# Kernel optimization log

Measured on AMD Instinct MI355X. Metric: run time of the kernel, lower is better.

Reference implementation:

```python
import jax, jax.numpy as jnp
import numpy as np

N = 100000
E = 1600000
F_IN = 128
HID = 64


def setup_inputs() -> dict:
    key = jax.random.key(0)
    ks = jax.random.split(key, 8)
    x = jax.random.normal(ks[0], (N, F_IN), dtype=jnp.float32)
    edge_index = jax.random.randint(ks[1], (2, E), 0, N, dtype=jnp.int32)
    # GCNConv params: weight [in, out] (glorot-ish scale), bias [out]
    W1 = jax.random.normal(ks[2], (F_IN, HID), dtype=jnp.float32) / np.sqrt(F_IN)
    b1 = jnp.zeros((HID,), dtype=jnp.float32)
    W2 = jax.random.normal(ks[3], (HID, HID), dtype=jnp.float32) / np.sqrt(HID)
    b2 = jnp.zeros((HID,), dtype=jnp.float32)
    Wc = jax.random.normal(ks[4], (HID, 1), dtype=jnp.float32) / np.sqrt(HID)
    bc = jnp.zeros((1,), dtype=jnp.float32)
    return {"x": x, "edge_index": edge_index, "W1": W1, "b1": b1,
            "W2": W2, "b2": b2, "Wc": Wc, "bc": bc}


def _gcn_conv(x, src, dst, W, b):
    # PyG GCNConv: h = x @ W, then symmetric-normalized aggregation over
    # edges with self-loops: out[d] = sum_e deg^-1/2[s] deg^-1/2[d] h[s] + b
    n = x.shape[0]
    h = x @ W                                            # [N, out]
    deg = jax.ops.segment_sum(jnp.ones_like(dst, dtype=h.dtype), dst,
                              num_segments=n)            # in-degree incl. self-loops
    dinv = jnp.where(deg > 0, jax.lax.rsqrt(deg), 0.0)   # [N]
    norm = dinv[src] * dinv[dst]                         # [E+N]
    msg = h[src] * norm[:, None]                         # gather + scale
    out = jax.ops.segment_sum(msg, dst, num_segments=n)  # scatter-add
    return out + b


def reference(x, edge_index, W1, b1, W2, b2, Wc, bc):
    n = x.shape[0]
    loop = jnp.arange(n, dtype=edge_index.dtype)
    src = jnp.concatenate([edge_index[0], loop])  # add self-loops
    dst = jnp.concatenate([edge_index[1], loop])
    h = jax.nn.relu(_gcn_conv(x, src, dst, W1, b1))  # dropout in eval mode = identity
    h = jax.nn.relu(_gcn_conv(h, src, dst, W2, b2))
    return (h @ Wc + bc).squeeze(-1)  # [N]
```

## Files before the change

### kernel.cpp

```cpp
#include <hip/hip_runtime.h>


#define FIN 128
#define HIDDEN 64
#define NBUCK 196
#define CAP 9216
#define EPB 8192

typedef __attribute__((ext_vector_type(8))) short bf16x8;
typedef __attribute__((ext_vector_type(4))) float f32x4;

__device__ __forceinline__ unsigned f2bf_pair(float a, float b) {
    unsigned ua = __float_as_uint(a);
    unsigned ub = __float_as_uint(b);
    ua = (ua + 0x7FFFu + ((ua >> 16) & 1u)) >> 16;
    ub = (ub + 0x7FFFu + ((ub >> 16) & 1u)) & 0xFFFF0000u;
    return ua | ub;
}
__device__ __forceinline__ unsigned short f2bf1(float a) {
    unsigned u = __float_as_uint(a);
    return (unsigned short)((u + 0x7FFFu + ((u >> 16) & 1u)) >> 16);
}
#define BF_LO(u) __uint_as_float((u) << 16)
#define BF_HI(u) __uint_as_float((u) & 0xFFFF0000u)

__global__ __launch_bounds__(256) void k_scatter_direct(const int* __restrict__ src,
                                                        const int* __restrict__ dst,
                                                        int* __restrict__ bcursor,
                                                        int* __restrict__ pairs, int e) {
    __shared__ int h[NBUCK], base_s[NBUCK], cur[NBUCK];
    int tid = threadIdx.x;
    if (tid < NBUCK) { h[tid] = 0; cur[tid] = 0; }
    __syncthreads();
    int start = blockIdx.x * EPB;
#pragma unroll
    for (int i = 0; i < EPB / 256; i++) {
        int idx = start + tid + i * 256;
        if (idx < e) atomicAdd(&h[dst[idx] >> 9], 1);
    }
    __syncthreads();
    if (tid < NBUCK && h[tid] > 0) base_s[tid] = atomicAdd(&bcursor[tid], h[tid]);
    __syncthreads();
#pragma unroll
    for (int i = 0; i < EPB / 256; i++) {
        int idx = start + tid + i * 256;
        if (idx < e) {
            int d = dst[idx];
            int b = d >> 9;
            int pos = base_s[b] + atomicAdd(&cur[b], 1);
            if (pos < CAP) pairs[b * CAP + pos] = (src[idx] << 9) | (d & 511);
        }
    }
}

__global__ __launch_bounds__(256) void k_csr_bucket(const int* __restrict__ pairs,
                                                    const int* __restrict__ bcursor,
                                                    int2* __restrict__ rowinfo,
                                                    float* __restrict__ dinv,
                                                    int* __restrict__ csr_src, int n) {
    __shared__ int cnt[512];
    __shared__ int off[512];
    __shared__ int ws2[256];
    int tid = threadIdx.x;
    int b = blockIdx.x;
    int node0 = b << 9;
    cnt[tid] = 0; cnt[tid + 256] = 0;
    __syncthreads();
    int s0 = b * CAP;
    int s1 = s0 + min(bcursor[b], CAP);
    for (int i = s0 + tid; i < s1; i += 256) atomicAdd(&cnt[pairs[i] & 511], 1);
    __syncthreads();
    int c0 = cnt[2 * tid], c1 = cnt[2 * tid + 1];
    int tsum = c0 + c1;
    ws2[tid] = tsum;
    __syncthreads();
    for (int o = 1; o < 256; o <<= 1) {
        int x = 0;
        if (tid >= o) x = ws2[tid - o];
        __syncthreads();
        if (tid >= o) ws2[tid] += x;
        __syncthreads();
    }
    int excl = ws2[tid] - tsum;
    off[2 * tid] = excl;
    off[2 * tid + 1] = excl + c0;
    int n0 = node0 + 2 * tid, n1 = node0 + 2 * tid + 1;
    if (n0 < n) { rowinfo[n0] = make_int2(s0 + excl, c0);      dinv[n0] = rsqrtf((float)c0 + 1.0f); }
    if (n1 < n) { rowinfo[n1] = make_int2(s0 + excl + c0, c1); dinv[n1] = rsqrtf((float)c1 + 1.0f); }
    cnt[2 * tid] = 0; cnt[2 * tid + 1] = 0;
    __syncthreads();
    for (int i = s0 + tid; i < s1; i += 256) {
        int p = pairs[i];
        int l = p & 511;
        int pos = s0 + off[l] + atomicAdd(&cnt[l], 1);
        csr_src[pos] = p >> 9;
    }
}


__global__ __launch_bounds__(256) void k_mfma1(const float4* __restrict__ x4,
                                               const float* __restrict__ w1,
                                               const float* __restrict__ dinv,
                                               uint2* __restrict__ hsb, int n) {
    __shared__ unsigned short sW[64 * 136];
    int tid = threadIdx.x;
#pragma unroll
    for (int i = 0; i < 32; i++) {
        int idx = tid + i * 256;
        int k = idx >> 6, ch = idx & 63;
        sW[ch * 136 + k] = f2bf1(w1[idx]);
    }
    __syncthreads();
    int lane = tid & 63, wave = tid >> 6;
    int quad = lane >> 4, nl = lane & 15;
    int node = blockIdx.x * 64 + wave * 16 + nl;
    int ic = min(node, n - 1);
    const float4* px = x4 + (size_t)ic * 32 + quad * 2;
    bf16x8 bfr[4];
#pragma unroll
    for (int kc = 0; kc < 4; kc++) {
        float4 p = px[kc * 8];
        float4 q = px[kc * 8 + 1];
        union { unsigned u[4]; bf16x8 v; } t;
        t.u[0] = f2bf_pair(p.x, p.y); t.u[1] = f2bf_pair(p.z, p.w);
        t.u[2] = f2bf_pair(q.x, q.y); t.u[3] = f2bf_pair(q.z, q.w);
        bfr[kc] = t.v;
    }
    const bf16x8* sW8 = (const bf16x8*)sW;
    f32x4 a0 = {0.f, 0.f, 0.f, 0.f}, a1 = a0, a2 = a0, a3 = a0;
#pragma unroll
    for (int kc = 0; kc < 4; kc++) {
        int ko = kc * 4 + quad;
        bf16x8 w0 = sW8[(nl +  0) * 17 + ko];
        bf16x8 w1f = sW8[(nl + 16) * 17 + ko];
        bf16x8 w2f = sW8[(nl + 32) * 17 + ko];
        bf16x8 w3f = sW8[(nl + 48) * 17 + ko];
        a0 = __builtin_amdgcn_mfma_f32_16x16x32_bf16(w0,  bfr[kc], a0, 0, 0, 0);
        a1 = __builtin_amdgcn_mfma_f32_16x16x32_bf16(w1f, bfr[kc], a1, 0, 0, 0);
        a2 = __builtin_amdgcn_mfma_f32_16x16x32_bf16(w2f, bfr[kc], a2, 0, 0, 0);
        a3 = __builtin_amdgcn_mfma_f32_16x16x32_bf16(w3f, bfr[kc], a3, 0, 0, 0);
    }
    if (node < n) {
        float s = dinv[node];
        uint2* o = hsb + (size_t)node * 16 + quad;
        o[0]  = make_uint2(f2bf_pair(a0.x * s, a0.y * s), f2bf_pair(a0.z * s, a0.w * s));
        o[4]  = make_uint2(f2bf_pair(a1.x * s, a1.y * s), f2bf_pair(a1.z * s, a1.w * s));
        o[8]  = make_uint2(f2bf_pair(a2.x * s, a2.y * s), f2bf_pair(a2.z * s, a2.w * s));
        o[12] = make_uint2(f2bf_pair(a3.x * s, a3.y * s), f2bf_pair(a3.z * s, a3.w * s));
    }
}

__global__ __launch_bounds__(256) void k_mfma2(const float4* __restrict__ v4,
                                               const float* __restrict__ w2,
                                               const float* __restrict__ dinv,
                                               uint2* __restrict__ hsb, int n) {
    __shared__ unsigned short sW[64 * 72];
    int tid = threadIdx.x;
#pragma unroll
    for (int i = 0; i < 16; i++) {
        int idx = tid + i * 256;
        int k = idx >> 6, ch = idx & 63;
        sW[ch * 72 + k] = f2bf1(w2[idx]);
    }
    __syncthreads();
    int lane = tid & 63, wave = tid >> 6;
    int quad = lane >> 4, nl = lane & 15;
    int node = blockIdx.x * 64 + wave * 16 + nl;
    int ic = min(node, n - 1);
    const float4* px = v4 + (size_t)ic * 16 + quad * 2;
    bf16x8 bfr[2];
#pragma unroll
    for (int kc = 0; kc < 2; kc++) {
        float4 p = px[kc * 8];
        float4 q = px[kc * 8 + 1];
        union { unsigned u[4]; bf16x8 v; } t;
        t.u[0] = f2bf_pair(p.x, p.y); t.u[1] = f2bf_pair(p.z, p.w);
        t.u[2] = f2bf_pair(q.x, q.y); t.u[3] = f2bf_pair(q.z, q.w);
        bfr[kc] = t.v;
    }
    const bf16x8* sW8 = (const bf16x8*)sW;
    f32x4 a0 = {0.f, 0.f, 0.f, 0.f}, a1 = a0, a2 = a0, a3 = a0;
#pragma unroll
    for (int kc = 0; kc < 2; kc++) {
        int ko = kc * 4 + quad;
        bf16x8 w0 = sW8[(nl +  0) * 9 + ko];
        bf16x8 w1f = sW8[(nl + 16) * 9 + ko];
        bf16x8 w2f = sW8[(nl + 32) * 9 + ko];
        bf16x8 w3f = sW8[(nl + 48) * 9 + ko];
        a0 = __builtin_amdgcn_mfma_f32_16x16x32_bf16(w0,  bfr[kc], a0, 0, 0, 0);
        a1 = __builtin_amdgcn_mfma_f32_16x16x32_bf16(w1f, bfr[kc], a1, 0, 0, 0);
        a2 = __builtin_amdgcn_mfma_f32_16x16x32_bf16(w2f, bfr[kc], a2, 0, 0, 0);
        a3 = __builtin_amdgcn_mfma_f32_16x16x32_bf16(w3f, bfr[kc], a3, 0, 0, 0);
    }
    if (node < n) {
        float s = dinv[node];
        uint2* o = hsb + (size_t)node * 16 + quad;
        o[0]  = make_uint2(f2bf_pair(a0.x * s, a0.y * s), f2bf_pair(a0.z * s, a0.w * s));
        o[4]  = make_uint2(f2bf_pair(a1.x * s, a1.y * s), f2bf_pair(a1.z * s, a1.w * s));
        o[8]  = make_uint2(f2bf_pair(a2.x * s, a2.y * s), f2bf_pair(a2.z * s, a2.w * s));
        o[12] = make_uint2(f2bf_pair(a3.x * s, a3.y * s), f2bf_pair(a3.z * s, a3.w * s));
    }
}

__global__ __launch_bounds__(256) void k_agg1_fin(const int2* __restrict__ rowinfo,
                                                  const int* __restrict__ csr_src,
                                                  const uint4* __restrict__ hsb4,
                                                  const float* __restrict__ dinv,
                                                  const float4* __restrict__ b1_4,
                                                  float4* __restrict__ v4out, int n) {
    int wid = (blockIdx.x * 256 + threadIdx.x) >> 6;
    int lane = threadIdx.x & 63;
    if (wid >= n) return;
    int el = lane >> 3, cq = lane & 7;
    int2 rpd = rowinfo[wid];
    int start = rpd.x, deg = rpd.y;
    int end = start + deg;
    float4 accA = make_float4(0.f, 0.f, 0.f, 0.f), accB = accA;
    if (deg > 0) {
        int rounds = (deg + 15) >> 4;
        for (int r = 0; r < rounds; r++) {
            int e0 = start + (r << 4) + el;
            int e1 = e0 + 8;
            int s0 = csr_src[min(e0, end - 1)];
            int s1 = csr_src[min(e1, end - 1)];
            float m0 = (e0 < end) ? 1.f : 0.f;
            float m1 = (e1 < end) ? 1.f : 0.f;
            uint4 g0 = hsb4[(size_t)s0 * 8 + cq];
            uint4 g1 = hsb4[(size_t)s1 * 8 + cq];
            accA.x += m0 * BF_LO(g0.x) + m1 * BF_LO(g1.x);
            accA.y += m0 * BF_HI(g0.x) + m1 * BF_HI(g1.x);
            accA.z += m0 * BF_LO(g0.y) + m1 * BF_LO(g1.y);
            accA.w += m0 * BF_HI(g0.y) + m1 * BF_HI(g1.y);
            accB.x += m0 * BF_LO(g0.z) + m1 * BF_LO(g1.z);
            accB.y += m0 * BF_HI(g0.z) + m1 * BF_HI(g1.z);
            accB.z += m0 * BF_LO(g0.w) + m1 * BF_LO(g1.w);
            accB.w += m0 * BF_HI(g0.w) + m1 * BF_HI(g1.w);
        }
    }
#pragma unroll
    for (int off = 8; off < 64; off <<= 1) {
        accA.x += __shfl_xor(accA.x, off); accA.y += __shfl_xor(accA.y, off);
        accA.z += __shfl_xor(accA.z, off); accA.w += __shfl_xor(accA.w, off);
        accB.x += __shfl_xor(accB.x, off); accB.y += __shfl_xor(accB.y, off);
        accB.z += __shfl_xor(accB.z, off); accB.w += __shfl_xor(accB.w, off);
    }
    if (el == 0) {
        uint4 g = hsb4[(size_t)wid * 8 + cq];
        float s = dinv[wid];
        float4 bA = b1_4[cq * 2], bB = b1_4[cq * 2 + 1];
        float4 vA, vB;
        vA.x = fmaxf(s * (accA.x + BF_LO(g.x)) + bA.x, 0.f);
        vA.y = fmaxf(s * (accA.y + BF_HI(g.x)) + bA.y, 0.f);
        vA.z = fmaxf(s * (accA.z + BF_LO(g.y)) + bA.z, 0.f);
        vA.w = fmaxf(s * (accA.w + BF_HI(g.y)) + bA.w, 0.f);
        vB.x = fmaxf(s * (accB.x + BF_LO(g.z)) + bB.x, 0.f);
        vB.y = fmaxf(s * (accB.y + BF_HI(g.z)) + bB.y, 0.f);
        vB.z = fmaxf(s * (accB.z + BF_LO(g.w)) + bB.z, 0.f);
        vB.w = fmaxf(s * (accB.w + BF_HI(g.w)) + bB.w, 0.f);
        v4out[(size_t)wid * 16 + cq * 2] = vA;
        v4out[(size_t)wid * 16 + cq * 2 + 1] = vB;
    }
}

__global__ __launch_bounds__(256) void k_agg2_head(const int2* __restrict__ rowinfo,
                                                   const int* __restrict__ csr_src,
                                                   const uint4* __restrict__ hsb4,
                                                   const float* __restrict__ dinv,
                                                   const float4* __restrict__ b2_4,
                                                   const float4* __restrict__ wc_4,
                                                   const float* __restrict__ bc,
                                                   float* __restrict__ out, int n) {
    int wid = (blockIdx.x * 256 + threadIdx.x) >> 6;
    int lane = threadIdx.x & 63;
    if (wid >= n) return;
    int el = lane >> 3, cq = lane & 7;
    int2 rpd = rowinfo[wid];
    int start = rpd.x, deg = rpd.y;
    int end = start + deg;
    float4 accA = make_float4(0.f, 0.f, 0.f, 0.f), accB = accA;
    if (deg > 0) {
        int rounds = (deg + 15) >> 4;
        for (int r = 0; r < rounds; r++) {
            int e0 = start + (r << 4) + el;
            int e1 = e0 + 8;
            int s0 = csr_src[min(e0, end - 1)];
            int s1 = csr_src[min(e1, end - 1)];
            float m0 = (e0 < end) ? 1.f : 0.f;
            float m1 = (e1 < end) ? 1.f : 0.f;
            uint4 g0 = hsb4[(size_t)s0 * 8 + cq];
            uint4 g1 = hsb4[(size_t)s1 * 8 + cq];
            accA.x += m0 * BF_LO(g0.x) + m1 * BF_LO(g1.x);
            accA.y += m0 * BF_HI(g0.x) + m1 * BF_HI(g1.x);
            accA.z += m0 * BF_LO(g0.y) + m1 * BF_LO(g1.y);
            accA.w += m0 * BF_HI(g0.y) + m1 * BF_HI(g1.y);
            accB.x += m0 * BF_LO(g0.z) + m1 * BF_LO(g1.z);
            accB.y += m0 * BF_HI(g0.z) + m1 * BF_HI(g1.z);
            accB.z += m0 * BF_LO(g0.w) + m1 * BF_LO(g1.w);
            accB.w += m0 * BF_HI(g0.w) + m1 * BF_HI(g1.w);
        }
    }
#pragma unroll
    for (int off = 8; off < 64; off <<= 1) {
        accA.x += __shfl_xor(accA.x, off); accA.y += __shfl_xor(accA.y, off);
        accA.z += __shfl_xor(accA.z, off); accA.w += __shfl_xor(accA.w, off);
        accB.x += __shfl_xor(accB.x, off); accB.y += __shfl_xor(accB.y, off);
        accB.z += __shfl_xor(accB.z, off); accB.w += __shfl_xor(accB.w, off);
    }
    uint4 g = hsb4[(size_t)wid * 8 + cq];
    float s = dinv[wid];
    float4 bA = b2_4[cq * 2], bB = b2_4[cq * 2 + 1];
    float4 wA = wc_4[cq * 2], wB = wc_4[cq * 2 + 1];
    float t = fmaxf(s * (accA.x + BF_LO(g.x)) + bA.x, 0.f) * wA.x
            + fmaxf(s * (accA.y + BF_HI(g.x)) + bA.y, 0.f) * wA.y
            + fmaxf(s * (accA.z + BF_LO(g.y)) + bA.z, 0.f) * wA.z
            + fmaxf(s * (accA.w + BF_HI(g.y)) + bA.w, 0.f) * wA.w
            + fmaxf(s * (accB.x + BF_LO(g.z)) + bB.x, 0.f) * wB.x
            + fmaxf(s * (accB.y + BF_HI(g.z)) + bB.y, 0.f) * wB.y
            + fmaxf(s * (accB.z + BF_LO(g.w)) + bB.z, 0.f) * wB.z
            + fmaxf(s * (accB.w + BF_HI(g.w)) + bB.w, 0.f) * wB.w;
    t += __shfl_xor(t, 1);
    t += __shfl_xor(t, 2);
    t += __shfl_xor(t, 4);
    if (lane == 0) out[wid] = t + bc[0];
}

extern "C" void kernel_launch(void* const* d_in, const int* in_sizes, int n_in,
                              void* d_out, int out_size, void* d_ws, size_t ws_size,
                              hipStream_t stream) {
    const float* x  = (const float*)d_in[0];
    const int*   ei = (const int*)d_in[1];
    const float* W1 = (const float*)d_in[2];
    const float* b1 = (const float*)d_in[3];
    const float* W2 = (const float*)d_in[4];
    const float* b2 = (const float*)d_in[5];
    const float* Wc = (const float*)d_in[6];
    const float* bc = (const float*)d_in[7];
    int n = in_sizes[0] / FIN;
    int e = in_sizes[1] / 2;
    const int* srcv = ei;
    const int* dstv = ei + e;

    char* ws = (char*)d_ws;
    float* dinv    = (float*)(ws + 0);
    int2*  rowinfo = (int2*)(ws + (512u << 10));
    int*   csr_src = (int*)(ws + 1536u * 1024);
    int*   bcursor = (int*)(ws + 8800u * 1024);
    uint2* hsb     = (uint2*)(ws + (9u << 20));
    float* v       = (float*)(ws + (22u << 20));
    int*   pairs   = (int*)v;

    int nb_sc   = (e + EPB - 1) / EPB;
    int nb_rows = (n + 63) / 64;
    int nb_wave = (n * 64 + 255) / 256;

    hipMemsetAsync(bcursor, 0, NBUCK * sizeof(int), stream);
    k_scatter_direct<<<nb_sc, 256, 0, stream>>>(srcv, dstv, bcursor, pairs, e);
    k_csr_bucket<<<NBUCK, 256, 0, stream>>>(pairs, bcursor, rowinfo, dinv, csr_src, n);

    k_mfma1<<<nb_rows, 256, 0, stream>>>((const float4*)x, W1, dinv, hsb, n);
    k_agg1_fin<<<nb_wave, 256, 0, stream>>>(rowinfo, csr_src, (const uint4*)hsb,
                                            dinv, (const float4*)b1, (float4*)v, n);
    k_mfma2<<<nb_rows, 256, 0, stream>>>((const float4*)v, W2, dinv, hsb, n);
    k_agg2_head<<<nb_wave, 256, 0, stream>>>(rowinfo, csr_src, (const uint4*)hsb,
                                             dinv, (const float4*)b2, (const float4*)Wc,
                                             bc, (float*)d_out, n);
}
```

Measured before the change: 257.8 us.

## Map four nodes per wavefront in aggregation kernels with 16 lanes per node

Changes both aggregation kernels from one 64-lane wave per destination node to 16 lanes per node (2 edge slots × 8 feature chunks), packing four nodes per wave. This is meant to cut the masked-out lanes and the multi-level shuffle reduction that were wasted on average-degree nodes, and to launch a quarter as many blocks. In exchange each node's edge loop runs more serial rounds with less memory-level parallelism per node, and high-degree nodes cause divergence within a wave.

```diff
diff --git a/kernel.cpp b/kernel.cpp
--- a/kernel.cpp
+++ b/kernel.cpp
@@ -208,45 +208,41 @@
                                                   const float* __restrict__ dinv,
                                                   const float4* __restrict__ b1_4,
                                                   float4* __restrict__ v4out, int n) {
-    int wid = (blockIdx.x * 256 + threadIdx.x) >> 6;
     int lane = threadIdx.x & 63;
-    if (wid >= n) return;
-    int el = lane >> 3, cq = lane & 7;
-    int2 rpd = rowinfo[wid];
+    int node = (blockIdx.x * 256 + threadIdx.x) >> 4;
+    if (node >= n) return;
+    int el = (lane >> 3) & 1, cq = lane & 7;
+    int2 rpd = rowinfo[node];
     int start = rpd.x, deg = rpd.y;
     int end = start + deg;
     float4 accA = make_float4(0.f, 0.f, 0.f, 0.f), accB = accA;
-    if (deg > 0) {
-        int rounds = (deg + 15) >> 4;
-        for (int r = 0; r < rounds; r++) {
-            int e0 = start + (r << 4) + el;
-            int e1 = e0 + 8;
-            int s0 = csr_src[min(e0, end - 1)];
-            int s1 = csr_src[min(e1, end - 1)];
-            float m0 = (e0 < end) ? 1.f : 0.f;
-            float m1 = (e1 < end) ? 1.f : 0.f;
-            uint4 g0 = hsb4[(size_t)s0 * 8 + cq];
-            uint4 g1 = hsb4[(size_t)s1 * 8 + cq];
-            accA.x += m0 * BF_LO(g0.x) + m1 * BF_LO(g1.x);
-            accA.y += m0 * BF_HI(g0.x) + m1 * BF_HI(g1.x);
-            accA.z += m0 * BF_LO(g0.y) + m1 * BF_LO(g1.y);
-            accA.w += m0 * BF_HI(g0.y) + m1 * BF_HI(g1.y);
-            accB.x += m0 * BF_LO(g0.z) + m1 * BF_LO(g1.z);
-            accB.y += m0 * BF_HI(g0.z) + m1 * BF_HI(g1.z);
-            accB.z += m0 * BF_LO(g0.w) + m1 * BF_LO(g1.w);
-            accB.w += m0 * BF_HI(g0.w) + m1 * BF_HI(g1.w);
-        }
-    }
-#pragma unroll
-    for (int off = 8; off < 64; off <<= 1) {
-        accA.x += __shfl_xor(accA.x, off); accA.y += __shfl_xor(accA.y, off);
-        accA.z += __shfl_xor(accA.z, off); accA.w += __shfl_xor(accA.w, off);
-        accB.x += __shfl_xor(accB.x, off); accB.y += __shfl_xor(accB.y, off);
-        accB.z += __shfl_xor(accB.z, off); accB.w += __shfl_xor(accB.w, off);
-    }
+    int nr = (deg + 3) >> 2;
+    for (int r = 0; r < nr; r++) {
+        int base = start + (r << 2);
+        int e0 = base + el;
+        int e1 = base + 2 + el;
+        int s0 = csr_src[min(e0, end - 1)];
+        int s1 = csr_src[min(e1, end - 1)];
+        float m0 = (e0 < end) ? 1.f : 0.f;
+        float m1 = (e1 < end) ? 1.f : 0.f;
+        uint4 g0 = hsb4[(size_t)s0 * 8 + cq];
+        uint4 g1 = hsb4[(size_t)s1 * 8 + cq];
+        accA.x += m0 * BF_LO(g0.x) + m1 * BF_LO(g1.x);
+        accA.y += m0 * BF_HI(g0.x) + m1 * BF_HI(g1.x);
+        accA.z += m0 * BF_LO(g0.y) + m1 * BF_LO(g1.y);
+        accA.w += m0 * BF_HI(g0.y) + m1 * BF_HI(g1.y);
+        accB.x += m0 * BF_LO(g0.z) + m1 * BF_LO(g1.z);
+        accB.y += m0 * BF_HI(g0.z) + m1 * BF_HI(g1.z);
+        accB.z += m0 * BF_LO(g0.w) + m1 * BF_LO(g1.w);
+        accB.w += m0 * BF_HI(g0.w) + m1 * BF_HI(g1.w);
+    }
+    accA.x += __shfl_xor(accA.x, 8); accA.y += __shfl_xor(accA.y, 8);
+    accA.z += __shfl_xor(accA.z, 8); accA.w += __shfl_xor(accA.w, 8);
+    accB.x += __shfl_xor(accB.x, 8); accB.y += __shfl_xor(accB.y, 8);
+    accB.z += __shfl_xor(accB.z, 8); accB.w += __shfl_xor(accB.w, 8);
     if (el == 0) {
-        uint4 g = hsb4[(size_t)wid * 8 + cq];
-        float s = dinv[wid];
+        uint4 g = hsb4[(size_t)node * 8 + cq];
+        float s = dinv[node];
         float4 bA = b1_4[cq * 2], bB = b1_4[cq * 2 + 1];
         float4 vA, vB;
         vA.x = fmaxf(s * (accA.x + BF_LO(g.x)) + bA.x, 0.f);
@@ -257,8 +253,8 @@
         vB.y = fmaxf(s * (accB.y + BF_HI(g.z)) + bB.y, 0.f);
         vB.z = fmaxf(s * (accB.z + BF_LO(g.w)) + bB.z, 0.f);
         vB.w = fmaxf(s * (accB.w + BF_HI(g.w)) + bB.w, 0.f);
-        v4out[(size_t)wid * 16 + cq * 2] = vA;
-        v4out[(size_t)wid * 16 + cq * 2 + 1] = vB;
+        v4out[(size_t)node * 16 + cq * 2] = vA;
+        v4out[(size_t)node * 16 + cq * 2 + 1] = vB;
     }
 }
 
@@ -270,44 +266,40 @@
                                                    const float4* __restrict__ wc_4,
                                                    const float* __restrict__ bc,
                                                    float* __restrict__ out, int n) {
-    int wid = (blockIdx.x * 256 + threadIdx.x) >> 6;
     int lane = threadIdx.x & 63;
-    if (wid >= n) return;
-    int el = lane >> 3, cq = lane & 7;
-    int2 rpd = rowinfo[wid];
+    int node = (blockIdx.x * 256 + threadIdx.x) >> 4;
+    if (node >= n) return;
+    int el = (lane >> 3) & 1, cq = lane & 7;
+    int2 rpd = rowinfo[node];
     int start = rpd.x, deg = rpd.y;
     int end = start + deg;
     float4 accA = make_float4(0.f, 0.f, 0.f, 0.f), accB = accA;
-    if (deg > 0) {
-        int rounds = (deg + 15) >> 4;
-        for (int r = 0; r < rounds; r++) {
-            int e0 = start + (r << 4) + el;
-            int e1 = e0 + 8;
-            int s0 = csr_src[min(e0, end - 1)];
-            int s1 = csr_src[min(e1, end - 1)];
-            float m0 = (e0 < end) ? 1.f : 0.f;
-            float m1 = (e1 < end) ? 1.f : 0.f;
-            uint4 g0 = hsb4[(size_t)s0 * 8 + cq];
-            uint4 g1 = hsb4[(size_t)s1 * 8 + cq];
-            accA.x += m0 * BF_LO(g0.x) + m1 * BF_LO(g1.x);
-            accA.y += m0 * BF_HI(g0.x) + m1 * BF_HI(g1.x);
-            accA.z += m0 * BF_LO(g0.y) + m1 * BF_LO(g1.y);
-            accA.w += m0 * BF_HI(g0.y) + m1 * BF_HI(g1.y);
-            accB.x += m0 * BF_LO(g0.z) + m1 * BF_LO(g1.z);
-            accB.y += m0 * BF_HI(g0.z) + m1 * BF_HI(g1.z);
-            accB.z += m0 * BF_LO(g0.w) + m1 * BF_LO(g1.w);
-            accB.w += m0 * BF_HI(g0.w) + m1 * BF_HI(g1.w);
-        }
-    }
-#pragma unroll
-    for (int off = 8; off < 64; off <<= 1) {
-        accA.x += __shfl_xor(accA.x, off); accA.y += __shfl_xor(accA.y, off);
-        accA.z += __shfl_xor(accA.z, off); accA.w += __shfl_xor(accA.w, off);
-        accB.x += __shfl_xor(accB.x, off); accB.y += __shfl_xor(accB.y, off);
-        accB.z += __shfl_xor(accB.z, off); accB.w += __shfl_xor(accB.w, off);
-    }
-    uint4 g = hsb4[(size_t)wid * 8 + cq];
-    float s = dinv[wid];
+    int nr = (deg + 3) >> 2;
+    for (int r = 0; r < nr; r++) {
+        int base = start + (r << 2);
+        int e0 = base + el;
+        int e1 = base + 2 + el;
+        int s0 = csr_src[min(e0, end - 1)];
+        int s1 = csr_src[min(e1, end - 1)];
+        float m0 = (e0 < end) ? 1.f : 0.f;
+        float m1 = (e1 < end) ? 1.f : 0.f;
+        uint4 g0 = hsb4[(size_t)s0 * 8 + cq];
+        uint4 g1 = hsb4[(size_t)s1 * 8 + cq];
+        accA.x += m0 * BF_LO(g0.x) + m1 * BF_LO(g1.x);
+        accA.y += m0 * BF_HI(g0.x) + m1 * BF_HI(g1.x);
+        accA.z += m0 * BF_LO(g0.y) + m1 * BF_LO(g1.y);
+        accA.w += m0 * BF_HI(g0.y) + m1 * BF_HI(g1.y);
+        accB.x += m0 * BF_LO(g0.z) + m1 * BF_LO(g1.z);
+        accB.y += m0 * BF_HI(g0.z) + m1 * BF_HI(g1.z);
+        accB.z += m0 * BF_LO(g0.w) + m1 * BF_LO(g1.w);
+        accB.w += m0 * BF_HI(g0.w) + m1 * BF_HI(g1.w);
+    }
+    accA.x += __shfl_xor(accA.x, 8); accA.y += __shfl_xor(accA.y, 8);
+    accA.z += __shfl_xor(accA.z, 8); accA.w += __shfl_xor(accA.w, 8);
+    accB.x += __shfl_xor(accB.x, 8); accB.y += __shfl_xor(accB.y, 8);
+    accB.z += __shfl_xor(accB.z, 8); accB.w += __shfl_xor(accB.w, 8);
+    uint4 g = hsb4[(size_t)node * 8 + cq];
+    float s = dinv[node];
     float4 bA = b2_4[cq * 2], bB = b2_4[cq * 2 + 1];
     float4 wA = wc_4[cq * 2], wB = wc_4[cq * 2 + 1];
     float t = fmaxf(s * (accA.x + BF_LO(g.x)) + bA.x, 0.f) * wA.x
@@ -321,7 +313,7 @@
     t += __shfl_xor(t, 1);
     t += __shfl_xor(t, 2);
     t += __shfl_xor(t, 4);
-    if (lane == 0) out[wid] = t + bc[0];
+    if ((lane & 15) == 0) out[node] = t + bc[0];
 }
 
 extern "C" void kernel_launch(void* const* d_in, const int* in_sizes, int n_in,
@@ -351,17 +343,17 @@
 
     int nb_sc   = (e + EPB - 1) / EPB;
     int nb_rows = (n + 63) / 64;
-    int nb_wave = (n * 64 + 255) / 256;
+    int nb_agg  = (n + 15) / 16;
 
     hipMemsetAsync(bcursor, 0, NBUCK * sizeof(int), stream);
     k_scatter_direct<<<nb_sc, 256, 0, stream>>>(srcv, dstv, bcursor, pairs, e);
     k_csr_bucket<<<NBUCK, 256, 0, stream>>>(pairs, bcursor, rowinfo, dinv, csr_src, n);
 
     k_mfma1<<<nb_rows, 256, 0, stream>>>((const float4*)x, W1, dinv, hsb, n);
-    k_agg1_fin<<<nb_wave, 256, 0, stream>>>(rowinfo, csr_src, (const uint4*)hsb,
-                                            dinv, (const float4*)b1, (float4*)v, n);
+    k_agg1_fin<<<nb_agg, 256, 0, stream>>>(rowinfo, csr_src, (const uint4*)hsb,
+                                           dinv, (const float4*)b1, (float4*)v, n);
     k_mfma2<<<nb_rows, 256, 0, stream>>>((const float4*)v, W2, dinv, hsb, n);
-    k_agg2_head<<<nb_wave, 256, 0, stream>>>(rowinfo, csr_src, (const uint4*)hsb,
-                                             dinv, (const float4*)b2, (const float4*)Wc,
-                                             bc, (float*)d_out, n);
-}
+    k_agg2_head<<<nb_agg, 256, 0, stream>>>(rowinfo, csr_src, (const uint4*)hsb,
+                                            dinv, (const float4*)b2, (const float4*)Wc,
+                                            bc, (float*)d_out, n);
+}
```

After: 233.7 us. 9.4% less time.
